# Performance work log

Measured on AMD Instinct MI355X. Metric: run time of the kernel, lower is better.

The kernel has to match this reference:

```python
import jax, jax.numpy as jnp
import numpy as np

N_NODES = 100000
N_EDGES = 1600000
IN_FEATS = 256
HEADS = 4
OUT_FEATS = 32


def setup_inputs() -> dict:
    key = jax.random.key(0)
    k1, k2, k3, k4, k5, k6 = jax.random.split(key, 6)
    feat = jax.random.normal(k1, (N_NODES, IN_FEATS), dtype=jnp.float32)
    fc_w = jax.random.normal(k2, (HEADS * OUT_FEATS, IN_FEATS), dtype=jnp.float32) * (1.0 / np.sqrt(IN_FEATS))
    attn_l = jax.random.normal(k3, (1, HEADS, OUT_FEATS), dtype=jnp.float32) * 0.1
    attn_r = jax.random.normal(k4, (1, HEADS, OUT_FEATS), dtype=jnp.float32) * 0.1
    src = jax.random.randint(k5, (N_EDGES,), 0, N_NODES, dtype=jnp.int32)
    dst = jax.random.randint(k6, (N_EDGES,), 0, N_NODES, dtype=jnp.int32)
    return {"feat": feat, "fc_w": fc_w, "attn_l": attn_l, "attn_r": attn_r, "src": src, "dst": dst}


def reference(feat, fc_w, attn_l, attn_r, src, dst):
    # feat: [N, F_in]; fc_w: [H*D, F_in]; attn_l/r: [1, H, D]; src/dst: [E]
    N = feat.shape[0]
    H, D = attn_l.shape[1], attn_l.shape[2]
    # linear projection (no bias), viewed as [N, H, D]
    ft = (feat @ fc_w.T).reshape(N, H, D)
    # per-node attention logits
    el = jnp.einsum('nhd,hd->nh', ft, attn_l[0])  # [N, H]
    er = jnp.einsum('nhd,hd->nh', ft, attn_r[0])  # [N, H]
    # per-edge score: leaky_relu(el[src] + er[dst])
    e = jax.nn.leaky_relu(el[src] + er[dst], negative_slope=0.2)  # [E, H]
    # edge softmax over incoming edges of each dst node (stable)
    emax = jax.ops.segment_max(e, dst, num_segments=N)  # [N, H]
    a = jnp.exp(e - emax[dst])  # [E, H]
    asum = jax.ops.segment_sum(a, dst, num_segments=N)  # [N, H]
    a = a / asum[dst]
    # attn_drop is a no-op in eval mode; weighted scatter-sum aggregation
    msg = ft[src] * a[:, :, None]  # [E, H, D]
    out = jax.ops.segment_sum(msg, dst, num_segments=N)  # [N, H, D]
    # final_layer=False, activation=None, norm=None -> flatten heads
    return out.reshape(N, H * D)
```

## Files before the change

kernel.cpp:

```cpp
#include <hip/hip_runtime.h>
#include <hip/hip_bf16.h>
#include <float.h>

#define IN_F 256
#define HD   128
#define NH   4
#define GM   128
#define CHUNK 8192
#define BNODES 256

typedef __bf16 bf16x8 __attribute__((ext_vector_type(8)));
typedef float  f32x4  __attribute__((ext_vector_type(4)));

__device__ __forceinline__ bf16x8 cvt8(const float4 a, const float4 b) {
    bf16x8 r;
    r[0] = (__bf16)a.x; r[1] = (__bf16)a.y; r[2] = (__bf16)a.z; r[3] = (__bf16)a.w;
    r[4] = (__bf16)b.x; r[5] = (__bf16)b.y; r[6] = (__bf16)b.z; r[7] = (__bf16)b.w;
    return r;
}

__global__ __launch_bounds__(256) void init_k(const float* __restrict__ w,
                                              __bf16* __restrict__ wfrag) {
    const int t = threadIdx.x;
    const int col = t >> 1;
    const int k0 = (t & 1) * 128;
    const int ct = col >> 4;
    const float* wp = w + (size_t)col * IN_F + k0;
#pragma unroll
    for (int kk = 0; kk < 128; kk += 8) {
        const float4 v0 = *(const float4*)(wp + kk);
        const float4 v1 = *(const float4*)(wp + kk + 4);
        const int k = k0 + kk;
        const int ks = k >> 5;
        const int lane = (col & 15) + (((k >> 3) & 3) << 4);
        *(bf16x8*)(wfrag + ((size_t)(ks * 8 + ct) * 64 + lane) * 8) = cvt8(v0, v1);
    }
}

__global__ __launch_bounds__(256) void gemm_fused(const float* __restrict__ feat,
                                                  const __bf16* __restrict__ wfrag,
                                                  const float* __restrict__ attn_l,
                                                  const float* __restrict__ attn_r,
                                                  const int* __restrict__ dst,
                                                  __bf16* __restrict__ ft,
                                                  float* __restrict__ el,
                                                  float* __restrict__ er,
                                                  int* __restrict__ cnt,
                                                  int N, int E,
                                                  int ntiles, int nbucket) {
    const int t = threadIdx.x;

    if (blockIdx.x >= ntiles) {
        __shared__ int cnt_l[512];
        const int c = blockIdx.x - ntiles;
        for (int j = t; j < nbucket; j += 256) cnt_l[j] = 0;
        __syncthreads();
        const int e0 = c * CHUNK;
#pragma unroll
        for (int k = 0; k < CHUNK / 256; ++k) {
            const int i = e0 + k * 256 + t;
            if (i < E) atomicAdd(&cnt_l[dst[i] >> 8], 1);
        }
        __syncthreads();
        for (int j = t; j < nbucket; j += 256) cnt[(size_t)c * nbucket + j] = cnt_l[j];
        return;
    }

    const int wv = t >> 6;
    const int lane = t & 63;
    const int frow = lane & 15;
    const int fq   = lane >> 4;

    float alw[8], arw[8];
#pragma unroll
    for (int ct = 0; ct < 8; ++ct) {
        alw[ct] = attn_l[ct * 16 + frow];
        arw[ct] = attn_r[ct * 16 + frow];
    }

    const int row0 = blockIdx.x * GM;
    const int r0 = row0 + wv * 32 + frow;
    const int r1 = r0 + 16;
    const bool ok0 = r0 < N;
    const bool ok1 = r1 < N;
    const float* fA0 = feat + (size_t)r0 * IN_F + fq * 8;
    const float* fA1 = feat + (size_t)r1 * IN_F + fq * 8;
    const __bf16* wfl = wfrag + (size_t)lane * 8;

    f32x4 acc[2][8];
#pragma unroll
    for (int mt = 0; mt < 2; ++mt)
#pragma unroll
        for (int ct = 0; ct < 8; ++ct) acc[mt][ct] = {0.f, 0.f, 0.f, 0.f};

#pragma unroll
    for (int ks = 0; ks < 8; ++ks) {
        bf16x8 af0, af1;
        if (ok0) {
            const float4 a = *(const float4*)(fA0 + ks * 32);
            const float4 b = *(const float4*)(fA0 + ks * 32 + 4);
            af0 = cvt8(a, b);
        } else {
#pragma unroll
            for (int i = 0; i < 8; ++i) af0[i] = (__bf16)0.f;
        }
        if (ok1) {
            const float4 a = *(const float4*)(fA1 + ks * 32);
            const float4 b = *(const float4*)(fA1 + ks * 32 + 4);
            af1 = cvt8(a, b);
        } else {
#pragma unroll
            for (int i = 0; i < 8; ++i) af1[i] = (__bf16)0.f;
        }
#pragma unroll
        for (int ct = 0; ct < 8; ++ct) {
            const bf16x8 bfrag = *(const bf16x8*)(wfl + (size_t)(ks * 8 + ct) * 512);
            acc[0][ct] = __builtin_amdgcn_mfma_f32_16x16x32_bf16(af0, bfrag, acc[0][ct], 0, 0, 0);
            acc[1][ct] = __builtin_amdgcn_mfma_f32_16x16x32_bf16(af1, bfrag, acc[1][ct], 0, 0, 0);
        }
    }

    const int rb = row0 + wv * 32 + (lane >> 4) * 4;
    if (row0 + GM <= N) {
#pragma unroll
        for (int mt = 0; mt < 2; ++mt)
#pragma unroll
            for (int ct = 0; ct < 8; ++ct)
#pragma unroll
                for (int reg = 0; reg < 4; ++reg) {
                    const int m = rb + mt * 16 + reg;
                    ft[(size_t)m * HD + ct * 16 + frow] = (__bf16)acc[mt][ct][reg];
                }
    } else {
#pragma unroll
        for (int mt = 0; mt < 2; ++mt)
#pragma unroll
            for (int ct = 0; ct < 8; ++ct)
#pragma unroll
                for (int reg = 0; reg < 4; ++reg) {
                    const int m = rb + mt * 16 + reg;
                    if (m < N) ft[(size_t)m * HD + ct * 16 + frow] = (__bf16)acc[mt][ct][reg];
                }
    }

#pragma unroll
    for (int mt = 0; mt < 2; ++mt) {
#pragma unroll
        for (int reg = 0; reg < 4; ++reg) {
            float pl[4], pr[4];
#pragma unroll
            for (int h = 0; h < 4; ++h) {
                const float v0 = acc[mt][2 * h][reg];
                const float v1 = acc[mt][2 * h + 1][reg];
                pl[h] = v0 * alw[2 * h] + v1 * alw[2 * h + 1];
                pr[h] = v0 * arw[2 * h] + v1 * arw[2 * h + 1];
            }
#pragma unroll
            for (int s = 1; s < 16; s <<= 1) {
#pragma unroll
                for (int h = 0; h < 4; ++h) {
                    pl[h] += __shfl_xor(pl[h], s);
                    pr[h] += __shfl_xor(pr[h], s);
                }
            }
            if (frow == 0) {
                const int r = row0 + wv * 32 + mt * 16 + (lane >> 4) * 4 + reg;
                if (r < N) {
                    *(float4*)(el + (size_t)r * NH) = make_float4(pl[0], pl[1], pl[2], pl[3]);
                    *(float4*)(er + (size_t)r * NH) = make_float4(pr[0], pr[1], pr[2], pr[3]);
                }
            }
        }
    }
}

__global__ __launch_bounds__(256) void chunkscan_k(int* __restrict__ cnt,
                                                   int* __restrict__ total,
                                                   int nchunk, int nbucket) {
    __shared__ int lds[256];
    const int b = blockIdx.x;
    const int t = threadIdx.x;
    const int x = (t < nchunk) ? cnt[(size_t)t * nbucket + b] : 0;
    lds[t] = x;
    __syncthreads();
    int v = x;
    for (int s = 1; s < 256; s <<= 1) {
        const int add = (t >= s) ? lds[t - s] : 0;
        __syncthreads();
        v += add;
        lds[t] = v;
        __syncthreads();
    }
    if (t < nchunk) cnt[(size_t)t * nbucket + b] = v - x;
    if (t == 255) total[b] = v;
}

__global__ __launch_bounds__(512) void bscatter_k(const int* __restrict__ src,
                                                  const int* __restrict__ dst,
                                                  const int* __restrict__ cnt,
                                                  const int* __restrict__ total,
                                                  int2* __restrict__ epair,
                                                  int E, int nbucket) {
    __shared__ int lds[512];
    __shared__ int cur[512];
    const int c = blockIdx.x;
    const int t = threadIdx.x;
    const int x = (t < nbucket) ? total[t] : 0;
    lds[t] = x;
    __syncthreads();
    int v = x;
    for (int s = 1; s < 512; s <<= 1) {
        const int add = (t >= s) ? lds[t - s] : 0;
        __syncthreads();
        v += add;
        lds[t] = v;
        __syncthreads();
    }
    const int cb = (t < nbucket) ? cnt[(size_t)c * nbucket + t] : 0;
    cur[t] = (v - x) + cb;
    __syncthreads();

    const int e0 = c * CHUNK;
#pragma unroll
    for (int k = 0; k < CHUNK / 512; ++k) {
        const int i = e0 + k * 512 + t;
        if (i < E) {
            const int d = dst[i];
            const int p = atomicAdd(&cur[d >> 8], 1);
            epair[p] = make_int2(src[i], d);
        }
    }
}

__global__ __launch_bounds__(512) void csr_k(const int2* __restrict__ epair,
                                             const int* __restrict__ total,
                                             int* __restrict__ deg,
                                             int* __restrict__ off,
                                             int* __restrict__ ssrc,
                                             int N, int nbucket) {
    __shared__ int lds[512];
    __shared__ int cl[256];
    __shared__ int lcur[256];
    const int b = blockIdx.x;
    const int t = threadIdx.x;

    const int x = (t < nbucket) ? total[t] : 0;
    lds[t] = x;
    __syncthreads();
    int v = x;
    for (int s = 1; s < 512; s <<= 1) {
        const int add = (t >= s) ? lds[t - s] : 0;
        __syncthreads();
        v += add;
        lds[t] = v;
        __syncthreads();
    }
    const int tb   = total[b];
    const int seg0 = lds[b] - tb;
    __syncthreads();

    if (t < 256) cl[t] = 0;
    __syncthreads();
    for (int i = seg0 + t; i < seg0 + tb; i += 512)
        atomicAdd(&cl[epair[i].y & 255], 1);
    __syncthreads();

    const int x2 = (t < 256) ? cl[t] : 0;
    lds[t] = x2;
    __syncthreads();
    int v2 = x2;
    for (int s = 1; s < 512; s <<= 1) {
        const int add = (t >= s) ? lds[t - s] : 0;
        __syncthreads();
        v2 += add;
        lds[t] = v2;
        __syncthreads();
    }
    const int loff = v2 - x2;
    if (t < 256) {
        const int node = b * BNODES + t;
        if (node < N) {
            deg[node] = x2;
            off[node] = seg0 + loff;
        }
        lcur[t] = loff;
    }
    __syncthreads();

    for (int i = seg0 + t; i < seg0 + tb; i += 512) {
        const int2 e = epair[i];
        const int p = atomicAdd(&lcur[e.y & 255], 1);
        ssrc[seg0 + p] = e.x;
    }
}

__global__ __launch_bounds__(64) void aggregate_k(const __bf16* __restrict__ ft,
                                                  const float* __restrict__ el,
                                                  const float* __restrict__ er,
                                                  const int* __restrict__ deg,
                                                  const int* __restrict__ off,
                                                  const int* __restrict__ ssrc,
                                                  float* __restrict__ out, int N) {
    const int n = blockIdx.x;
    const int lane = threadIdx.x;
    const int il = lane & 15;
    const int q  = lane >> 4;
    const int h  = il >> 2;
    float4* outp = (float4*)(out + (size_t)n * HD);
    const int dn = deg[n];
    if (dn == 0) {
        if (q < 2) outp[il * 2 + q] = make_float4(0.f, 0.f, 0.f, 0.f);
        return;
    }
    const int start = off[n];
    const float4 er4 = *(const float4*)(er + (size_t)n * NH);

    __shared__ float a_lds[64 * NH];
    __shared__ int   s_lds[64];
    float4 ssum = make_float4(0.f, 0.f, 0.f, 0.f);
    float acc[8];
#pragma unroll
    for (int i = 0; i < 8; ++i) acc[i] = 0.f;

    for (int c0 = 0; c0 < dn; c0 += 64) {
        const int j = c0 + lane;
        float4 a = make_float4(0.f, 0.f, 0.f, 0.f);
        int sv = 0;
        if (j < dn) {
            sv = ssrc[start + j];
            float4 e = *(const float4*)(el + (size_t)sv * NH);
            e.x += er4.x; e.y += er4.y; e.z += er4.z; e.w += er4.w;
            e.x = e.x >= 0.f ? e.x : 0.2f * e.x;
            e.y = e.y >= 0.f ? e.y : 0.2f * e.y;
            e.z = e.z >= 0.f ? e.z : 0.2f * e.z;
            e.w = e.w >= 0.f ? e.w : 0.2f * e.w;
            a.x = __expf(e.x); a.y = __expf(e.y);
            a.z = __expf(e.z); a.w = __expf(e.w);
            ssum.x += a.x; ssum.y += a.y; ssum.z += a.z; ssum.w += a.w;
        }
        s_lds[lane] = sv;
        *(float4*)(a_lds + lane * NH) = a;
        __syncthreads();
        const int cnt2 = min(64, dn - c0);
        for (int j2 = 0; j2 < cnt2; j2 += 8) {
            const int e0 = j2 + q;
            const int e1 = j2 + 4 + q;
            const int sv0 = s_lds[e0];
            const int sv1 = s_lds[e1];
            const float a0 = a_lds[e0 * NH + h];
            const float a1 = a_lds[e1 * NH + h];
            const bf16x8 f0 = *(const bf16x8*)(ft + (size_t)sv0 * HD + il * 8);
            const bf16x8 f1 = *(const bf16x8*)(ft + (size_t)sv1 * HD + il * 8);
#pragma unroll
            for (int k = 0; k < 8; ++k) acc[k] = fmaf(a0, (float)f0[k], acc[k]);
#pragma unroll
            for (int k = 0; k < 8; ++k) acc[k] = fmaf(a1, (float)f1[k], acc[k]);
        }
        __syncthreads();
    }
#pragma unroll
    for (int s = 1; s < 64; s <<= 1) {
        ssum.x += __shfl_xor(ssum.x, s);
        ssum.y += __shfl_xor(ssum.y, s);
        ssum.z += __shfl_xor(ssum.z, s);
        ssum.w += __shfl_xor(ssum.w, s);
    }
#pragma unroll
    for (int k = 0; k < 8; ++k) {
        acc[k] += __shfl_xor(acc[k], 16);
        acc[k] += __shfl_xor(acc[k], 32);
    }
    const float sumh = (h == 0) ? ssum.x : (h == 1) ? ssum.y : (h == 2) ? ssum.z : ssum.w;
    const float inv = 1.f / sumh;
    if (q < 2) {
        const int b = q * 4;
        outp[il * 2 + q] = make_float4(acc[b] * inv, acc[b + 1] * inv,
                                       acc[b + 2] * inv, acc[b + 3] * inv);
    }
}

extern "C" void kernel_launch(void* const* d_in, const int* in_sizes, int n_in,
                              void* d_out, int out_size, void* d_ws, size_t ws_size,
                              hipStream_t stream) {
    const float* feat   = (const float*)d_in[0];
    const float* fc_w   = (const float*)d_in[1];
    const float* attn_l = (const float*)d_in[2];
    const float* attn_r = (const float*)d_in[3];
    const int*   src    = (const int*)d_in[4];
    const int*   dst    = (const int*)d_in[5];
    const int N = in_sizes[0] / IN_F;
    const int E = in_sizes[4];
    float* out = (float*)d_out;

    const int ntiles  = (N + GM - 1) / GM;
    const int nchunk  = (E + CHUNK - 1) / CHUNK;
    const int nbucket = (N + BNODES - 1) / BNODES;

    char* wp = (char*)d_ws;
    __bf16* ft = (__bf16*)wp; wp += (size_t)N * HD * 2;
    float* el  = (float*)wp; wp += (size_t)N * NH * 4;
    float* er  = (float*)wp; wp += (size_t)N * NH * 4;
    int* deg   = (int*)wp;   wp += (size_t)N * 4;
    int* off   = (int*)wp;   wp += (size_t)N * 4;
    int* cnt   = (int*)wp;   wp += (size_t)nchunk * nbucket * 4;
    int* total = (int*)wp;   wp += (size_t)nbucket * 4 + 64;
    int* ssrc  = (int*)wp;   wp += (size_t)E * 4;
    int2* epair = (int2*)wp; wp += (size_t)E * 8;
    __bf16* wfrag = (__bf16*)wp; wp += (size_t)HD * IN_F * 2;

    init_k<<<dim3(1), dim3(256), 0, stream>>>(fc_w, wfrag);
    gemm_fused<<<dim3(ntiles + nchunk), dim3(256), 0, stream>>>(
        feat, wfrag, attn_l, attn_r, dst, ft, el, er, cnt, N, E, ntiles, nbucket);
    chunkscan_k<<<dim3(nbucket), dim3(256), 0, stream>>>(cnt, total, nchunk, nbucket);
    bscatter_k<<<dim3(nchunk), dim3(512), 0, stream>>>(src, dst, cnt, total, epair, E, nbucket);
    csr_k<<<dim3(nbucket), dim3(512), 0, stream>>>(epair, total, deg, off, ssrc, N, nbucket);
    aggregate_k<<<dim3(N), dim3(64), 0, stream>>>(ft, el, er, deg, off, ssrc, out, N);
}
```

Baseline: 330.8 us.

## Fuse CSR build phases into GEMM kernel with grid-wide sub-barriers

Merges the GEMM, chunk count, chunk scan, bucket scatter and per-bucket CSR kernels into one launch. A dedicated set of blocks runs the CSR phases, separated by atomic spin barriers, while the remaining blocks do the GEMM tiles concurrently. Bucket start offsets now come from atomic allocation instead of a global prefix scan, so bucket order in memory is nondeterministic but each bucket stays contiguous. The change removes three kernel launches and lets graph preprocessing overlap the projection. The spin barriers assume all NCSR blocks are co-resident, which risks deadlock if the GEMM blocks are scheduled first and fill the device.

```diff
diff --git a/kernel.cpp b/kernel.cpp
--- a/kernel.cpp
+++ b/kernel.cpp
@@ -8,6 +8,7 @@
 #define GM   128
 #define CHUNK 8192
 #define BNODES 256
+#define NCSR 242
 
 typedef __bf16 bf16x8 __attribute__((ext_vector_type(8)));
 typedef float  f32x4  __attribute__((ext_vector_type(4)));
@@ -20,8 +21,10 @@
 }
 
 __global__ __launch_bounds__(256) void init_k(const float* __restrict__ w,
-                                              __bf16* __restrict__ wfrag) {
+                                              __bf16* __restrict__ wfrag,
+                                              int* __restrict__ ctrl) {
     const int t = threadIdx.x;
+    if (t < 2) ctrl[t] = 0;
     const int col = t >> 1;
     const int k0 = (t & 1) * 128;
     const int ct = col >> 4;
@@ -37,32 +40,135 @@
     }
 }
 
-__global__ __launch_bounds__(256) void gemm_fused(const float* __restrict__ feat,
-                                                  const __bf16* __restrict__ wfrag,
-                                                  const float* __restrict__ attn_l,
-                                                  const float* __restrict__ attn_r,
-                                                  const int* __restrict__ dst,
-                                                  __bf16* __restrict__ ft,
-                                                  float* __restrict__ el,
-                                                  float* __restrict__ er,
-                                                  int* __restrict__ cnt,
-                                                  int N, int E,
-                                                  int ntiles, int nbucket) {
+__device__ __forceinline__ void subbar(int* bar, int target) {
+    __syncthreads();
+    if (threadIdx.x == 0) {
+        __hip_atomic_fetch_add(bar, 1, __ATOMIC_ACQ_REL, __HIP_MEMORY_SCOPE_AGENT);
+        while (__hip_atomic_load(bar, __ATOMIC_RELAXED, __HIP_MEMORY_SCOPE_AGENT) < target)
+            __builtin_amdgcn_s_sleep(16);
+        (void)__hip_atomic_load(bar, __ATOMIC_ACQUIRE, __HIP_MEMORY_SCOPE_AGENT);
+    }
+    __syncthreads();
+}
+
+__global__ __launch_bounds__(256) void mega(const float* __restrict__ feat,
+                                            const __bf16* __restrict__ wfrag,
+                                            const float* __restrict__ attn_l,
+                                            const float* __restrict__ attn_r,
+                                            const int* __restrict__ src,
+                                            const int* __restrict__ dst,
+                                            __bf16* __restrict__ ft,
+                                            float* __restrict__ el,
+                                            float* __restrict__ er,
+                                            int* __restrict__ cnt,
+                                            int* __restrict__ total,
+                                            int* __restrict__ bstart,
+                                            int2* __restrict__ epair,
+                                            int* __restrict__ deg,
+                                            int* __restrict__ off,
+                                            int* __restrict__ ssrc,
+                                            int* __restrict__ ctrl,
+                                            int N, int E,
+                                            int ntiles, int nchunk, int nbucket) {
     const int t = threadIdx.x;
 
-    if (blockIdx.x >= ntiles) {
+    if (blockIdx.x < NCSR) {
         __shared__ int cnt_l[512];
-        const int c = blockIdx.x - ntiles;
-        for (int j = t; j < nbucket; j += 256) cnt_l[j] = 0;
-        __syncthreads();
-        const int e0 = c * CHUNK;
-#pragma unroll
-        for (int k = 0; k < CHUNK / 256; ++k) {
-            const int i = e0 + k * 256 + t;
-            if (i < E) atomicAdd(&cnt_l[dst[i] >> 8], 1);
-        }
-        __syncthreads();
-        for (int j = t; j < nbucket; j += 256) cnt[(size_t)c * nbucket + j] = cnt_l[j];
+        __shared__ int sl[256];
+        __shared__ int cl[256];
+        __shared__ int lcur[256];
+        const int cid = blockIdx.x;
+        int* bar  = ctrl;
+        int* gcur = ctrl + 1;
+
+        for (int c = cid; c < nchunk; c += NCSR) {
+            for (int j = t; j < nbucket; j += 256) cnt_l[j] = 0;
+            __syncthreads();
+            const int e0 = c * CHUNK;
+#pragma unroll
+            for (int k = 0; k < CHUNK / 256; ++k) {
+                const int i = e0 + k * 256 + t;
+                if (i < E) atomicAdd(&cnt_l[dst[i] >> 8], 1);
+            }
+            __syncthreads();
+            for (int j = t; j < nbucket; j += 256) cnt[(size_t)c * nbucket + j] = cnt_l[j];
+            __syncthreads();
+        }
+        subbar(bar, NCSR * 1);
+
+        for (int b = cid; b < nbucket; b += NCSR) {
+            const int x = (t < nchunk) ? cnt[(size_t)t * nbucket + b] : 0;
+            sl[t] = x;
+            __syncthreads();
+            int v = x;
+            for (int s = 1; s < 256; s <<= 1) {
+                const int add = (t >= s) ? sl[t - s] : 0;
+                __syncthreads();
+                v += add;
+                sl[t] = v;
+                __syncthreads();
+            }
+            if (t < nchunk) cnt[(size_t)t * nbucket + b] = v - x;
+            if (t == 255) {
+                total[b] = v;
+                bstart[b] = atomicAdd(gcur, v);
+            }
+            __syncthreads();
+        }
+        subbar(bar, NCSR * 2);
+
+        for (int c = cid; c < nchunk; c += NCSR) {
+            for (int j = t; j < 512; j += 256)
+                cnt_l[j] = (j < nbucket) ? bstart[j] + cnt[(size_t)c * nbucket + j] : 0;
+            __syncthreads();
+            const int e0 = c * CHUNK;
+#pragma unroll
+            for (int k = 0; k < CHUNK / 256; ++k) {
+                const int i = e0 + k * 256 + t;
+                if (i < E) {
+                    const int d = dst[i];
+                    const int p = atomicAdd(&cnt_l[d >> 8], 1);
+                    epair[p] = make_int2(src[i], d);
+                }
+            }
+            __syncthreads();
+        }
+        subbar(bar, NCSR * 3);
+
+        for (int b = cid; b < nbucket; b += NCSR) {
+            const int seg0 = bstart[b];
+            const int tb   = total[b];
+            cl[t] = 0;
+            __syncthreads();
+            for (int i = seg0 + t; i < seg0 + tb; i += 256)
+                atomicAdd(&cl[epair[i].y & 255], 1);
+            __syncthreads();
+            const int x2 = cl[t];
+            sl[t] = x2;
+            __syncthreads();
+            int v2 = x2;
+            for (int s = 1; s < 256; s <<= 1) {
+                const int add = (t >= s) ? sl[t - s] : 0;
+                __syncthreads();
+                v2 += add;
+                sl[t] = v2;
+                __syncthreads();
+            }
+            const int loff = v2 - x2;
+            const int node = b * BNODES + t;
+            if (node < N) {
+                deg[node] = x2;
+                off[node] = seg0 + loff;
+            }
+            lcur[t] = loff;
+            __syncthreads();
+            for (int i = seg0 + t; i < seg0 + tb; i += 256) {
+                const int2 e = epair[i];
+                const int p = atomicAdd(&lcur[e.y & 255], 1);
+                ssrc[seg0 + p] = e.x;
+            }
+            __syncthreads();
+        }
         return;
     }
 
@@ -78,219 +184,102 @@
         arw[ct] = attn_r[ct * 16 + frow];
     }
 
-    const int row0 = blockIdx.x * GM;
-    const int r0 = row0 + wv * 32 + frow;
-    const int r1 = r0 + 16;
-    const bool ok0 = r0 < N;
-    const bool ok1 = r1 < N;
-    const float* fA0 = feat + (size_t)r0 * IN_F + fq * 8;
-    const float* fA1 = feat + (size_t)r1 * IN_F + fq * 8;
-    const __bf16* wfl = wfrag + (size_t)lane * 8;
-
-    f32x4 acc[2][8];
-#pragma unroll
-    for (int mt = 0; mt < 2; ++mt)
-#pragma unroll
-        for (int ct = 0; ct < 8; ++ct) acc[mt][ct] = {0.f, 0.f, 0.f, 0.f};
-
-#pragma unroll
-    for (int ks = 0; ks < 8; ++ks) {
-        bf16x8 af0, af1;
-        if (ok0) {
-            const float4 a = *(const float4*)(fA0 + ks * 32);
-            const float4 b = *(const float4*)(fA0 + ks * 32 + 4);
-            af0 = cvt8(a, b);
+    const int gstride = gridDim.x - NCSR;
+    for (int tile = blockIdx.x - NCSR; tile < ntiles; tile += gstride) {
+        const int row0 = tile * GM;
+        const int r0 = row0 + wv * 32 + frow;
+        const int r1 = r0 + 16;
+        const bool ok0 = r0 < N;
+        const bool ok1 = r1 < N;
+        const float* fA0 = feat + (size_t)r0 * IN_F + fq * 8;
+        const float* fA1 = feat + (size_t)r1 * IN_F + fq * 8;
+        const __bf16* wfl = wfrag + (size_t)lane * 8;
+
+        f32x4 acc[2][8];
+#pragma unroll
+        for (int mt = 0; mt < 2; ++mt)
+#pragma unroll
+            for (int ct = 0; ct < 8; ++ct) acc[mt][ct] = {0.f, 0.f, 0.f, 0.f};
+
+#pragma unroll
+        for (int ks = 0; ks < 8; ++ks) {
+            bf16x8 af0, af1;
+            if (ok0) {
+                const float4 a = *(const float4*)(fA0 + ks * 32);
+                const float4 b = *(const float4*)(fA0 + ks * 32 + 4);
+                af0 = cvt8(a, b);
+            } else {
+#pragma unroll
+                for (int i = 0; i < 8; ++i) af0[i] = (__bf16)0.f;
+            }
+            if (ok1) {
+                const float4 a = *(const float4*)(fA1 + ks * 32);
+                const float4 b = *(const float4*)(fA1 + ks * 32 + 4);
+                af1 = cvt8(a, b);
+            } else {
+#pragma unroll
+                for (int i = 0; i < 8; ++i) af1[i] = (__bf16)0.f;
+            }
+#pragma unroll
+            for (int ct = 0; ct < 8; ++ct) {
+                const bf16x8 bfrag = *(const bf16x8*)(wfl + (size_t)(ks * 8 + ct) * 512);
+                acc[0][ct] = __builtin_amdgcn_mfma_f32_16x16x32_bf16(af0, bfrag, acc[0][ct], 0, 0, 0);
+                acc[1][ct] = __builtin_amdgcn_mfma_f32_16x16x32_bf16(af1, bfrag, acc[1][ct], 0, 0, 0);
+            }
+        }
+
+        const int rb = row0 + wv * 32 + (lane >> 4) * 4;
+        if (row0 + GM <= N) {
+#pragma unroll
+            for (int mt = 0; mt < 2; ++mt)
+#pragma unroll
+                for (int ct = 0; ct < 8; ++ct)
+#pragma unroll
+                    for (int reg = 0; reg < 4; ++reg) {
+                        const int m = rb + mt * 16 + reg;
+                        ft[(size_t)m * HD + ct * 16 + frow] = (__bf16)acc[mt][ct][reg];
+                    }
         } else {
 #pragma unroll
-            for (int i = 0; i < 8; ++i) af0[i] = (__bf16)0.f;
-        }
-        if (ok1) {
-            const float4 a = *(const float4*)(fA1 + ks * 32);
-            const float4 b = *(const float4*)(fA1 + ks * 32 + 4);
-            af1 = cvt8(a, b);
-        } else {
-#pragma unroll
-            for (int i = 0; i < 8; ++i) af1[i] = (__bf16)0.f;
-        }
-#pragma unroll
-        for (int ct = 0; ct < 8; ++ct) {
-            const bf16x8 bfrag = *(const bf16x8*)(wfl + (size_t)(ks * 8 + ct) * 512);
-            acc[0][ct] = __builtin_amdgcn_mfma_f32_16x16x32_bf16(af0, bfrag, acc[0][ct], 0, 0, 0);
-            acc[1][ct] = __builtin_amdgcn_mfma_f32_16x16x32_bf16(af1, bfrag, acc[1][ct], 0, 0, 0);
-        }
-    }
-
-    const int rb = row0 + wv * 32 + (lane >> 4) * 4;
-    if (row0 + GM <= N) {
-#pragma unroll
-        for (int mt = 0; mt < 2; ++mt)
-#pragma unroll
-            for (int ct = 0; ct < 8; ++ct)
-#pragma unroll
-                for (int reg = 0; reg < 4; ++reg) {
-                    const int m = rb + mt * 16 + reg;
-                    ft[(size_t)m * HD + ct * 16 + frow] = (__bf16)acc[mt][ct][reg];
+            for (int mt = 0; mt < 2; ++mt)
+#pragma unroll
+                for (int ct = 0; ct < 8; ++ct)
+#pragma unroll
+                    for (int reg = 0; reg < 4; ++reg) {
+                        const int m = rb + mt * 16 + reg;
+                        if (m < N) ft[(size_t)m * HD + ct * 16 + frow] = (__bf16)acc[mt][ct][reg];
+                    }
+        }
+
+#pragma unroll
+        for (int mt = 0; mt < 2; ++mt) {
+#pragma unroll
+            for (int reg = 0; reg < 4; ++reg) {
+                float pl[4], pr[4];
+#pragma unroll
+                for (int h = 0; h < 4; ++h) {
+                    const float v0 = acc[mt][2 * h][reg];
+                    const float v1 = acc[mt][2 * h + 1][reg];
+                    pl[h] = v0 * alw[2 * h] + v1 * alw[2 * h + 1];
+                    pr[h] = v0 * arw[2 * h] + v1 * arw[2 * h + 1];
                 }
-    } else {
-#pragma unroll
-        for (int mt = 0; mt < 2; ++mt)
-#pragma unroll
-            for (int ct = 0; ct < 8; ++ct)
-#pragma unroll
-                for (int reg = 0; reg < 4; ++reg) {
-                    const int m = rb + mt * 16 + reg;
-                    if (m < N) ft[(size_t)m * HD + ct * 16 + frow] = (__bf16)acc[mt][ct][reg];
+#pragma unroll
+                for (int s = 1; s < 16; s <<= 1) {
+#pragma unroll
+                    for (int h = 0; h < 4; ++h) {
+                        pl[h] += __shfl_xor(pl[h], s);
+                        pr[h] += __shfl_xor(pr[h], s);
+                    }
                 }
-    }
-
-#pragma unroll
-    for (int mt = 0; mt < 2; ++mt) {
-#pragma unroll
-        for (int reg = 0; reg < 4; ++reg) {
-            float pl[4], pr[4];
-#pragma unroll
-            for (int h = 0; h < 4; ++h) {
-                const float v0 = acc[mt][2 * h][reg];
-                const float v1 = acc[mt][2 * h + 1][reg];
-                pl[h] = v0 * alw[2 * h] + v1 * alw[2 * h + 1];
-                pr[h] = v0 * arw[2 * h] + v1 * arw[2 * h + 1];
-            }
-#pragma unroll
-            for (int s = 1; s < 16; s <<= 1) {
-#pragma unroll
-                for (int h = 0; h < 4; ++h) {
-                    pl[h] += __shfl_xor(pl[h], s);
-                    pr[h] += __shfl_xor(pr[h], s);
+                if (frow == 0) {
+                    const int r = row0 + wv * 32 + mt * 16 + (lane >> 4) * 4 + reg;
+                    if (r < N) {
+                        *(float4*)(el + (size_t)r * NH) = make_float4(pl[0], pl[1], pl[2], pl[3]);
+                        *(float4*)(er + (size_t)r * NH) = make_float4(pr[0], pr[1], pr[2], pr[3]);
+                    }
                 }
             }
-            if (frow == 0) {
-                const int r = row0 + wv * 32 + mt * 16 + (lane >> 4) * 4 + reg;
-                if (r < N) {
-                    *(float4*)(el + (size_t)r * NH) = make_float4(pl[0], pl[1], pl[2], pl[3]);
-                    *(float4*)(er + (size_t)r * NH) = make_float4(pr[0], pr[1], pr[2], pr[3]);
-                }
-            }
-        }
-    }
-}
-
-__global__ __launch_bounds__(256) void chunkscan_k(int* __restrict__ cnt,
-                                                   int* __restrict__ total,
-                                                   int nchunk, int nbucket) {
-    __shared__ int lds[256];
-    const int b = blockIdx.x;
-    const int t = threadIdx.x;
-    const int x = (t < nchunk) ? cnt[(size_t)t * nbucket + b] : 0;
-    lds[t] = x;
-    __syncthreads();
-    int v = x;
-    for (int s = 1; s < 256; s <<= 1) {
-        const int add = (t >= s) ? lds[t - s] : 0;
-        __syncthreads();
-        v += add;
-        lds[t] = v;
-        __syncthreads();
-    }
-    if (t < nchunk) cnt[(size_t)t * nbucket + b] = v - x;
-    if (t == 255) total[b] = v;
-}
-
-__global__ __launch_bounds__(512) void bscatter_k(const int* __restrict__ src,
-                                                  const int* __restrict__ dst,
-                                                  const int* __restrict__ cnt,
-                                                  const int* __restrict__ total,
-                                                  int2* __restrict__ epair,
-                                                  int E, int nbucket) {
-    __shared__ int lds[512];
-    __shared__ int cur[512];
-    const int c = blockIdx.x;
-    const int t = threadIdx.x;
-    const int x = (t < nbucket) ? total[t] : 0;
-    lds[t] = x;
-    __syncthreads();
-    int v = x;
-    for (int s = 1; s < 512; s <<= 1) {
-        const int add = (t >= s) ? lds[t - s] : 0;
-        __syncthreads();
-        v += add;
-        lds[t] = v;
-        __syncthreads();
-    }
-    const int cb = (t < nbucket) ? cnt[(size_t)c * nbucket + t] : 0;
-    cur[t] = (v - x) + cb;
-    __syncthreads();
-
-    const int e0 = c * CHUNK;
-#pragma unroll
-    for (int k = 0; k < CHUNK / 512; ++k) {
-        const int i = e0 + k * 512 + t;
-        if (i < E) {
-            const int d = dst[i];
-            const int p = atomicAdd(&cur[d >> 8], 1);
-            epair[p] = make_int2(src[i], d);
-        }
-    }
-}
-
-__global__ __launch_bounds__(512) void csr_k(const int2* __restrict__ epair,
-                                             const int* __restrict__ total,
-                                             int* __restrict__ deg,
-                                             int* __restrict__ off,
-                                             int* __restrict__ ssrc,
-                                             int N, int nbucket) {
-    __shared__ int lds[512];
-    __shared__ int cl[256];
-    __shared__ int lcur[256];
-    const int b = blockIdx.x;
-    const int t = threadIdx.x;
-
-    const int x = (t < nbucket) ? total[t] : 0;
-    lds[t] = x;
-    __syncthreads();
-    int v = x;
-    for (int s = 1; s < 512; s <<= 1) {
-        const int add = (t >= s) ? lds[t - s] : 0;
-        __syncthreads();
-        v += add;
-        lds[t] = v;
-        __syncthreads();
-    }
-    const int tb   = total[b];
-    const int seg0 = lds[b] - tb;
-    __syncthreads();
-
-    if (t < 256) cl[t] = 0;
-    __syncthreads();
-    for (int i = seg0 + t; i < seg0 + tb; i += 512)
-        atomicAdd(&cl[epair[i].y & 255], 1);
-    __syncthreads();
-
-    const int x2 = (t < 256) ? cl[t] : 0;
-    lds[t] = x2;
-    __syncthreads();
-    int v2 = x2;
-    for (int s = 1; s < 512; s <<= 1) {
-        const int add = (t >= s) ? lds[t - s] : 0;
-        __syncthreads();
-        v2 += add;
-        lds[t] = v2;
-        __syncthreads();
-    }
-    const int loff = v2 - x2;
-    if (t < 256) {
-        const int node = b * BNODES + t;
-        if (node < N) {
-            deg[node] = x2;
-            off[node] = seg0 + loff;
-        }
-        lcur[t] = loff;
-    }
-    __syncthreads();
-
-    for (int i = seg0 + t; i < seg0 + tb; i += 512) {
-        const int2 e = epair[i];
-        const int p = atomicAdd(&lcur[e.y & 255], 1);
-        ssrc[seg0 + p] = e.x;
+        }
     }
 }
 
@@ -403,16 +392,17 @@
     int* deg   = (int*)wp;   wp += (size_t)N * 4;
     int* off   = (int*)wp;   wp += (size_t)N * 4;
     int* cnt   = (int*)wp;   wp += (size_t)nchunk * nbucket * 4;
-    int* total = (int*)wp;   wp += (size_t)nbucket * 4 + 64;
+    int* total = (int*)wp;   wp += 2048;
+    int* bstart= (int*)wp;   wp += 2048;
+    int* ctrl  = (int*)wp;   wp += 64;
     int* ssrc  = (int*)wp;   wp += (size_t)E * 4;
     int2* epair = (int2*)wp; wp += (size_t)E * 8;
     __bf16* wfrag = (__bf16*)wp; wp += (size_t)HD * IN_F * 2;
 
-    init_k<<<dim3(1), dim3(256), 0, stream>>>(fc_w, wfrag);
-    gemm_fused<<<dim3(ntiles + nchunk), dim3(256), 0, stream>>>(
-        feat, wfrag, attn_l, attn_r, dst, ft, el, er, cnt, N, E, ntiles, nbucket);
-    chunkscan_k<<<dim3(nbucket), dim3(256), 0, stream>>>(cnt, total, nchunk, nbucket);
-    bscatter_k<<<dim3(nchunk), dim3(512), 0, stream>>>(src, dst, cnt, total, epair, E, nbucket);
-    csr_k<<<dim3(nbucket), dim3(512), 0, stream>>>(epair, total, deg, off, ssrc, N, nbucket);
+    init_k<<<dim3(1), dim3(256), 0, stream>>>(fc_w, wfrag, ctrl);
+    mega<<<dim3(NCSR + ntiles), dim3(256), 0, stream>>>(
+        feat, wfrag, attn_l, attn_r, src, dst, ft, el, er,
+        cnt, total, bstart, epair, deg, off, ssrc, ctrl,
+        N, E, ntiles, nchunk, nbucket);
     aggregate_k<<<dim3(N), dim3(64), 0, stream>>>(ft, el, er, deg, off, ssrc, out, N);
 }
```

Measured after the change: 421.0 us. +27.3%, slower.
